# Performance work log

Measured on AMD Instinct MI355X. Metric: run time of the kernel, lower is better.

Reference implementation:

```python
import jax, jax.numpy as jnp
import numpy as np

A_COEF, B_COEF, C_COEF = 1.0, 0.1, 10.0
KL_COEF = 0.005
EPS = 1e-6

B, P1, F, P2 = 32, 778, 1538, 3000
PARAM_DIM, LATENT = 61, 64


def setup_inputs() -> dict:
    key = jax.random.key(0)
    ks = jax.random.split(key, 9)
    return {
        "recon_x": jax.random.normal(ks[0], (B, PARAM_DIM), jnp.float32),
        "x": jax.random.normal(ks[1], (B, PARAM_DIM), jnp.float32),
        "mu": jax.random.normal(ks[2], (B, LATENT), jnp.float32),
        "logvar": jax.random.normal(ks[3], (B, LATENT), jnp.float32),
        "recon_xyz": jax.random.normal(ks[4], (B, P1, 3), jnp.float32),
        "hand_xyz": jax.random.normal(ks[5], (B, P1, 3), jnp.float32),
        "hand_faces": jax.random.randint(ks[6], (B, F, 3), 0, P1, jnp.int64),
        "obj_pts": jax.random.normal(ks[7], (B, P2, 3), jnp.float32),
        "v_weights": jax.random.uniform(ks[8], (P1,), jnp.float32),
    }


def _verts_normals_single(verts, faces):
    # verts: (V,3), faces: (F,3). PyTorch3D-style area-weighted vertex normals.
    v0 = verts[faces[:, 0]]
    v1 = verts[faces[:, 1]]
    v2 = verts[faces[:, 2]]
    fn = jnp.cross(v1 - v0, v2 - v0)  # (F,3) ~ 2*area*face_normal
    n = (jnp.zeros_like(verts)
         .at[faces[:, 0]].add(fn)
         .at[faces[:, 1]].add(fn)
         .at[faces[:, 2]].add(fn))
    norm = jnp.linalg.norm(n, axis=-1, keepdims=True)
    return n / jnp.maximum(norm, EPS)


_verts_normals = jax.vmap(_verts_normals_single)


def _sqdist(xp, yp):
    # (B,P1,P2) pairwise squared distances
    x2 = jnp.sum(xp * xp, axis=-1)[:, :, None]
    y2 = jnp.sum(yp * yp, axis=-1)[:, None, :]
    return x2 + y2 - 2.0 * jnp.einsum('bpd,bqd->bpq', xp, yp)


def _point2point_signed(xp, yp, x_normals):
    # xp: (B,P1,3) hand, yp: (B,P2,3) object, x_normals: (B,P1,3)
    d2 = _sqdist(xp, yp)
    xidx = jnp.argmin(d2, axis=2)  # (B,P1) nearest object point per hand vert
    yidx = jnp.argmin(d2, axis=1)  # (B,P2) nearest hand vert per object point
    x_near = jnp.take_along_axis(yp, xidx[..., None], axis=1)  # (B,P1,3)
    y_near = jnp.take_along_axis(xp, yidx[..., None], axis=1)  # (B,P2,3)
    x2y = xp - x_near
    y2x = yp - y_near
    y_nn = jnp.take_along_axis(x_normals, yidx[..., None], axis=1)  # (B,P2,3)
    in_out = jnp.sign(jnp.sum(y_nn * y2x, axis=-1))
    y2x_signed = jnp.linalg.norm(y2x, axis=2) * in_out  # (B,P2)
    x2y_signed = jnp.linalg.norm(x2y, axis=2)           # (B,P1)
    return y2x_signed, x2y_signed


def _loss_cnet(verts_rhand, verts_rhand_gt, faces, verts_obj, v_weights):
    v_w2 = jnp.power(v_weights, 1.0 / 2.5)
    rh_n = _verts_normals(verts_rhand, faces)
    rh_n_gt = _verts_normals(verts_rhand_gt, faces)
    o2h, h2o = _point2point_signed(verts_rhand, verts_obj, rh_n)
    o2h_gt, h2o_gt = _point2point_signed(verts_rhand_gt, verts_obj, rh_n_gt)
    w_dist = (o2h_gt < 0.01) & (o2h_gt > -0.005)
    w_neg = o2h < 0.0
    w = jnp.where(w_neg, 1.5, jnp.where(w_dist, 1.0, 0.1))
    loss_h = 35.0 * (1.0 - KL_COEF) * jnp.mean(jnp.abs(jnp.abs(h2o) - jnp.abs(h2o_gt)) * v_w2)
    loss_o = 30.0 * (1.0 - KL_COEF) * jnp.mean(jnp.abs(o2h - o2h_gt) * w)
    return loss_h + loss_o


def reference(recon_x, x, mu, logvar, recon_xyz, hand_xyz, hand_faces, obj_pts, v_weights):
    bsz = recon_x.shape[0]
    param_loss = jnp.sum((recon_x - x) ** 2) / bsz
    recon_loss = jnp.sum((recon_xyz - hand_xyz) ** 2) / hand_xyz.shape[0]
    KLD = -0.5 * jnp.sum(1.0 + logvar - mu ** 2 - jnp.exp(logvar)) / hand_xyz.shape[0]
    cvae_loss = recon_loss + KLD
    ho_loss = _loss_cnet(recon_xyz, hand_xyz, hand_faces, obj_pts, v_weights)
    loss = A_COEF * cvae_loss + B_COEF * param_loss + C_COEF * ho_loss
    return loss, param_loss, ho_loss, recon_loss, KLD
```

## Files before the change

### kernel.cpp

```cpp
#include <hip/hip_runtime.h>
#include <math.h>

#define B 32
#define P1 778
#define NF 1538
#define P2 3000
#define PARAM_DIM 61
#define LATENT 64

#define NCH_O2H 4
#define CH_O2H 768
#define NCH_H2O 15
#define CH_H2O 200
#define RED1_BLKS 16
#define HC_BLKS 128
#define OC_BLKS 192
#define HALF_F 769

#define D1_NRM 128
#define D1_TOT (D1_NRM + RED1_BLKS)
#define D2_O2H (NCH_O2H * 64)
#define D2_H2O (NCH_H2O * 64)
#define D2_TOT (D2_O2H + D2_H2O)
#define D3_TOT (OC_BLKS + HC_BLKS)

#define NP_OFF  0
#define NP_SZ   (2*2*B*P1*4)
#define OS_OFF  (NP_OFF + NP_SZ)
#define OS_SZ   (2*B*P2)
#define HP_OFF  (OS_OFF + OS_SZ)
#define HP_SZ   (NCH_H2O*2*B*P1)
#define R1_OFF  (HP_OFF + HP_SZ)
#define RH_OFF  (R1_OFF + RED1_BLKS*3)
#define RO_OFF  (RH_OFF + HC_BLKS)

__global__ __launch_bounds__(256) void kd1(
    const float* __restrict__ recon_x, const float* __restrict__ x,
    const float* __restrict__ mu, const float* __restrict__ logvar,
    const float* __restrict__ recon_xyz, const float* __restrict__ hand_xyz,
    const int* __restrict__ faces, float* __restrict__ ws) {
  __shared__ float4 sv[P1];
  __shared__ float sn[4][2336];
  const int tid = threadIdx.x;
  const int bid = blockIdx.x;

  if (bid < D1_NRM) {
    const int half = bid >> 6, r = bid & 63, set = r >> 5, b = r & 31;
    const float* verts = (set == 0 ? recon_xyz : hand_xyz) + b * P1 * 3;
    const int* f = faces + b * NF * 3 + half * HALF_F * 3;
    const int nf = (half == 0) ? HALF_F : (NF - HALF_F);
    for (int i = tid; i < P1; i += 256)
      sv[i] = make_float4(verts[3*i], verts[3*i+1], verts[3*i+2], 0.f);
    for (int i = tid; i < 4 * 2336; i += 256) ((float*)sn)[i] = 0.f;
    __syncthreads();
    float* s = sn[tid >> 6];
    for (int k = tid; k < nf; k += 256) {
      int i0 = f[3*k], i1 = f[3*k+1], i2 = f[3*k+2];
      float4 v0 = sv[i0], v1 = sv[i1], v2 = sv[i2];
      float e0x = v1.x - v0.x, e0y = v1.y - v0.y, e0z = v1.z - v0.z;
      float e1x = v2.x - v0.x, e1y = v2.y - v0.y, e1z = v2.z - v0.z;
      float fx = e0y * e1z - e0z * e1y;
      float fy = e0z * e1x - e0x * e1z;
      float fz = e0x * e1y - e0y * e1x;
      atomicAdd(&s[3*i0+0], fx); atomicAdd(&s[3*i0+1], fy); atomicAdd(&s[3*i0+2], fz);
      atomicAdd(&s[3*i1+0], fx); atomicAdd(&s[3*i1+1], fy); atomicAdd(&s[3*i1+2], fz);
      atomicAdd(&s[3*i2+0], fx); atomicAdd(&s[3*i2+1], fy); atomicAdd(&s[3*i2+2], fz);
    }
    __syncthreads();
    float4* np = (float4*)(ws + NP_OFF) + (size_t)((half * 2 + set) * B + b) * P1;
    for (int p = tid; p < P1; p += 256) {
      float nx = sn[0][3*p] + sn[1][3*p] + sn[2][3*p] + sn[3][3*p];
      float ny = sn[0][3*p+1] + sn[1][3*p+1] + sn[2][3*p+1] + sn[3][3*p+1];
      float nz = sn[0][3*p+2] + sn[1][3*p+2] + sn[2][3*p+2] + sn[3][3*p+2];
      np[p] = make_float4(nx, ny, nz, 0.f);
    }
  } else {
    const int blk = bid - D1_NRM;
    const int gtid = blk * 256 + tid, stride = RED1_BLKS * 256;
    float sp = 0.f, sr = 0.f, sk = 0.f;
    for (int i = gtid; i < B * PARAM_DIM; i += stride) { float d = recon_x[i] - x[i]; sp += d * d; }
    for (int i = gtid; i < B * P1 * 3; i += stride)    { float d = recon_xyz[i] - hand_xyz[i]; sr += d * d; }
    for (int i = gtid; i < B * LATENT; i += stride)    { float lv = logvar[i], m = mu[i]; sk += 1.f + lv - m * m - expf(lv); }
    for (int off = 32; off > 0; off >>= 1) {
      sp += __shfl_down(sp, off, 64);
      sr += __shfl_down(sr, off, 64);
      sk += __shfl_down(sk, off, 64);
    }
    float* sred = (float*)sn;
    const int wv = tid >> 6;
    if ((tid & 63) == 0) { sred[wv*3] = sp; sred[wv*3+1] = sr; sred[wv*3+2] = sk; }
    __syncthreads();
    if (tid == 0) {
      float a = 0.f, bb = 0.f, c = 0.f;
      for (int w = 0; w < 4; ++w) { a += sred[w*3]; bb += sred[w*3+1]; c += sred[w*3+2]; }
      ws[R1_OFF + blk*3+0] = a; ws[R1_OFF + blk*3+1] = bb; ws[R1_OFF + blk*3+2] = c;
    }
  }
}

__global__ __launch_bounds__(256) void kd2(
    const float* __restrict__ recon_xyz, const float* __restrict__ hand_xyz,
    const float* __restrict__ obj, float* __restrict__ ws) {
  __shared__ float4 s4[P1];
  const int tid = threadIdx.x;
  const int bid = blockIdx.x;

  if (bid < D2_O2H) {
    const int chunk = bid >> 6, r = bid & 63, set = r >> 5, b = r & 31;
    const float* verts = (set == 0 ? recon_xyz : hand_xyz) + b * P1 * 3;
    for (int i = tid; i < P1; i += 256) {
      float vx = verts[3*i], vy = verts[3*i+1], vz = verts[3*i+2];
      s4[i] = make_float4(vx, vy, vz, vx*vx + vy*vy + vz*vz + 64.f);
    }
    __syncthreads();
    const int q0 = chunk * CH_O2H + tid;
    const int q1 = q0 + 256;
    const int q2 = q0 + 512;
    const bool act2 = q2 < P2;
    const float* op = obj + (size_t)b * P2 * 3;
    float p0x = op[3*q0], p0y = op[3*q0+1], p0z = op[3*q0+2];
    float p1x = op[3*q1], p1y = op[3*q1+1], p1z = op[3*q1+2];
    float p2x = 0.f, p2y = 0.f, p2z = 0.f;
    if (act2) { p2x = op[3*q2]; p2y = op[3*q2+1]; p2z = op[3*q2+2]; }
    const float a0 = -2.f*p0x, b0 = -2.f*p0y, c0 = -2.f*p0z;
    const float a1 = -2.f*p1x, b1 = -2.f*p1y, c1 = -2.f*p1z;
    const float a2 = -2.f*p2x, b2 = -2.f*p2y, c2 = -2.f*p2z;
    unsigned best0 = 0xFFFFFFFFu, best1 = 0xFFFFFFFFu, best2 = 0xFFFFFFFFu;
    #pragma unroll 4
    for (int p = 0; p < P1; p += 2) {
      float4 h0 = s4[p], h1 = s4[p+1];
      float d00 = fmaf(h0.x, a0, fmaf(h0.y, b0, fmaf(h0.z, c0, h0.w)));
      float d01 = fmaf(h1.x, a0, fmaf(h1.y, b0, fmaf(h1.z, c0, h1.w)));
      float d10 = fmaf(h0.x, a1, fmaf(h0.y, b1, fmaf(h0.z, c1, h0.w)));
      float d11 = fmaf(h1.x, a1, fmaf(h1.y, b1, fmaf(h1.z, c1, h1.w)));
      float d20 = fmaf(h0.x, a2, fmaf(h0.y, b2, fmaf(h0.z, c2, h0.w)));
      float d21 = fmaf(h1.x, a2, fmaf(h1.y, b2, fmaf(h1.z, c2, h1.w)));
      unsigned k00 = (__float_as_uint(d00) & 0xFFFFFC00u) | (unsigned)p;
      unsigned k01 = (__float_as_uint(d01) & 0xFFFFFC00u) | (unsigned)(p+1);
      unsigned k10 = (__float_as_uint(d10) & 0xFFFFFC00u) | (unsigned)p;
      unsigned k11 = (__float_as_uint(d11) & 0xFFFFFC00u) | (unsigned)(p+1);
      unsigned k20 = (__float_as_uint(d20) & 0xFFFFFC00u) | (unsigned)p;
      unsigned k21 = (__float_as_uint(d21) & 0xFFFFFC00u) | (unsigned)(p+1);
      unsigned n0 = k00 < k01 ? k00 : k01;
      unsigned n1 = k10 < k11 ? k10 : k11;
      unsigned n2 = k20 < k21 ? k20 : k21;
      best0 = n0 < best0 ? n0 : best0;
      best1 = n1 < best1 ? n1 : best1;
      best2 = n2 < best2 ? n2 : best2;
    }
    const float4* np0 = (const float4*)(ws + NP_OFF) + (size_t)(set * B + b) * P1;
    const float4* np1 = np0 + (size_t)2 * B * P1;
    float* os = ws + OS_OFF + (size_t)(set * B + b) * P2;
    {
      int bi = (int)(best0 & 1023u); bi = bi < P1 ? bi : P1 - 1;
      float4 h = s4[bi]; float4 na = np0[bi], nb = np1[bi];
      float nx = na.x + nb.x, ny = na.y + nb.y, nz = na.z + nb.z;
      float dx = p0x - h.x, dy = p0y - h.y, dz = p0z - h.z;
      float d2 = fmaf(dx, dx, fmaf(dy, dy, dz * dz));
      float dt = nx * dx + ny * dy + nz * dz;
      float sg = (dt > 0.f) ? 1.f : ((dt < 0.f) ? -1.f : 0.f);
      os[q0] = sqrtf(d2) * sg;
    }
    {
      int bi = (int)(best1 & 1023u); bi = bi < P1 ? bi : P1 - 1;
      float4 h = s4[bi]; float4 na = np0[bi], nb = np1[bi];
      float nx = na.x + nb.x, ny = na.y + nb.y, nz = na.z + nb.z;
      float dx = p1x - h.x, dy = p1y - h.y, dz = p1z - h.z;
      float d2 = fmaf(dx, dx, fmaf(dy, dy, dz * dz));
      float dt = nx * dx + ny * dy + nz * dz;
      float sg = (dt > 0.f) ? 1.f : ((dt < 0.f) ? -1.f : 0.f);
      os[q1] = sqrtf(d2) * sg;
    }
    if (act2) {
      int bi = (int)(best2 & 1023u); bi = bi < P1 ? bi : P1 - 1;
      float4 h = s4[bi]; float4 na = np0[bi], nb = np1[bi];
      float nx = na.x + nb.x, ny = na.y + nb.y, nz = na.z + nb.z;
      float dx = p2x - h.x, dy = p2y - h.y, dz = p2z - h.z;
      float d2 = fmaf(dx, dx, fmaf(dy, dy, dz * dz));
      float dt = nx * dx + ny * dy + nz * dz;
      float sg = (dt > 0.f) ? 1.f : ((dt < 0.f) ? -1.f : 0.f);
      os[q2] = sqrtf(d2) * sg;
    }

  } else {
    const int t = bid - D2_O2H;
    const int chunk = t >> 6, r = t & 63, set = r >> 5, b = r & 31;
    const float* verts = (set == 0 ? recon_xyz : hand_xyz) + b * P1 * 3;
    const float* op = obj + (size_t)(b * P2 + chunk * CH_H2O) * 3;
    for (int i = tid; i < CH_H2O; i += 256) {
      float ox = op[3*i], oy = op[3*i+1], oz = op[3*i+2];
      s4[i] = make_float4(ox, oy, oz, ox*ox + oy*oy + oz*oz);
    }
    __syncthreads();
    float* part = ws + HP_OFF + (size_t)((chunk * 2 + set) * B + b) * P1;
    const int p0 = tid, p1 = tid + 256, p2 = tid + 512;
    float ax = verts[3*p0], ay = verts[3*p0+1], az = verts[3*p0+2];
    float bx = verts[3*p1], by = verts[3*p1+1], bz = verts[3*p1+2];
    float cx = verts[3*p2], cy = verts[3*p2+1], cz = verts[3*p2+2];
    float h2a = ax*ax+ay*ay+az*az, h2b = bx*bx+by*by+bz*bz, h2c = cx*cx+cy*cy+cz*cz;
    float nax = -2.f*ax, nay = -2.f*ay, naz = -2.f*az;
    float nbx = -2.f*bx, nby = -2.f*by, nbz = -2.f*bz;
    float ncx = -2.f*cx, ncy = -2.f*cy, ncz = -2.f*cz;
    float m0 = 3.0e38f, m1 = 3.0e38f, m2 = 3.0e38f;
    #pragma unroll 4
    for (int qq = 0; qq < CH_H2O; ++qq) {
      float4 o = s4[qq];
      m0 = fminf(m0, fmaf(o.x, nax, fmaf(o.y, nay, fmaf(o.z, naz, o.w))));
      m1 = fminf(m1, fmaf(o.x, nbx, fmaf(o.y, nby, fmaf(o.z, nbz, o.w))));
      m2 = fminf(m2, fmaf(o.x, ncx, fmaf(o.y, ncy, fmaf(o.z, ncz, o.w))));
    }
    part[p0] = m0 + h2a;
    part[p1] = m1 + h2b;
    part[p2] = m2 + h2c;
    if (tid < P1 - 768) {
      const int p3 = 768 + tid;
      float tx = verts[3*p3], ty = verts[3*p3+1], tz = verts[3*p3+2];
      float h2t = tx*tx+ty*ty+tz*tz;
      float ntx = -2.f*tx, nty = -2.f*ty, ntz = -2.f*tz;
      float m3 = 3.0e38f;
      for (int qq = 0; qq < CH_H2O; ++qq) {
        float4 o = s4[qq];
        m3 = fminf(m3, fmaf(o.x, ntx, fmaf(o.y, nty, fmaf(o.z, ntz, o.w))));
      }
      part[p3] = m3 + h2t;
    }
  }
}

__global__ __launch_bounds__(256) void kd3(const float* __restrict__ vw,
                                           float* __restrict__ ws) {
  __shared__ float sred[4];
  const int tid = threadIdx.x;
  const int bid = blockIdx.x;
  if (bid < OC_BLKS) {
    const int gtid = bid * 256 + tid, stride = OC_BLKS * 256;
    float so = 0.f;
    for (int i = gtid; i < B * P2; i += stride) {
      float osA = ws[OS_OFF + i];
      float osB = ws[OS_OFF + (size_t)B * P2 + i];
      bool wdist = (osB < 0.01f) && (osB > -0.005f);
      float w = (osA < 0.f) ? 1.5f : (wdist ? 1.f : 0.1f);
      so += fabsf(osA - osB) * w;
    }
    for (int off = 32; off > 0; off >>= 1) so += __shfl_down(so, off, 64);
    if ((tid & 63) == 0) sred[tid >> 6] = so;
    __syncthreads();
    if (tid == 0) ws[RO_OFF + bid] = sred[0] + sred[1] + sred[2] + sred[3];
  } else {
    const int blk = bid - OC_BLKS;
    const int gtid = blk * 256 + tid, stride = HC_BLKS * 256;
    float sh = 0.f;
    for (int i = gtid; i < B * P1; i += stride) {
      const int p = i % P1;
      float m0 = 3.0e38f, m1 = 3.0e38f;
      #pragma unroll
      for (int c = 0; c < NCH_H2O; ++c) {
        m0 = fminf(m0, ws[HP_OFF + (size_t)(c*2+0) * B * P1 + i]);
        m1 = fminf(m1, ws[HP_OFF + (size_t)(c*2+1) * B * P1 + i]);
      }
      m0 = fmaxf(m0, 0.f); m1 = fmaxf(m1, 0.f);
      sh += fabsf(sqrtf(m0) - sqrtf(m1)) * powf(vw[p], 0.4f);
    }
    for (int off = 32; off > 0; off >>= 1) sh += __shfl_down(sh, off, 64);
    if ((tid & 63) == 0) sred[tid >> 6] = sh;
    __syncthreads();
    if (tid == 0) ws[RH_OFF + blk] = sred[0] + sred[1] + sred[2] + sred[3];
  }
}

__global__ void kfin(const float* __restrict__ ws, float* __restrict__ out) {
  const int lane = threadIdx.x;
  float sp = 0.f, sr = 0.f, sk = 0.f, sh = 0.f, so = 0.f;
  for (int i = lane; i < RED1_BLKS; i += 64) {
    sp += ws[R1_OFF + i*3+0]; sr += ws[R1_OFF + i*3+1]; sk += ws[R1_OFF + i*3+2];
  }
  for (int i = lane; i < HC_BLKS; i += 64) sh += ws[RH_OFF + i];
  for (int i = lane; i < OC_BLKS; i += 64) so += ws[RO_OFF + i];
  for (int off = 32; off > 0; off >>= 1) {
    sp += __shfl_down(sp, off, 64);
    sr += __shfl_down(sr, off, 64);
    sk += __shfl_down(sk, off, 64);
    sh += __shfl_down(sh, off, 64);
    so += __shfl_down(so, off, 64);
  }
  if (lane == 0) {
    float param_loss = sp / (float)B;
    float recon_loss = sr / (float)B;
    float KLD = -0.5f * sk / (float)B;
    float cvae = recon_loss + KLD;
    float loss_h = 35.f * (1.f - 0.005f) * sh / (float)(B * P1);
    float loss_o = 30.f * (1.f - 0.005f) * so / (float)(B * P2);
    float ho = loss_h + loss_o;
    out[0] = cvae + 0.1f * param_loss + 10.f * ho;
    out[1] = param_loss;
    out[2] = ho;
    out[3] = recon_loss;
    out[4] = KLD;
  }
}

extern "C" void kernel_launch(void* const* d_in, const int* in_sizes, int n_in,
                              void* d_out, int out_size, void* d_ws, size_t ws_size,
                              hipStream_t stream) {
  const float* recon_x   = (const float*)d_in[0];
  const float* x         = (const float*)d_in[1];
  const float* mu        = (const float*)d_in[2];
  const float* logvar    = (const float*)d_in[3];
  const float* recon_xyz = (const float*)d_in[4];
  const float* hand_xyz  = (const float*)d_in[5];
  const int*   faces     = (const int*)d_in[6];
  const float* obj       = (const float*)d_in[7];
  const float* vw        = (const float*)d_in[8];
  float* ws = (float*)d_ws;
  float* out = (float*)d_out;

  kd1<<<dim3(D1_TOT), 256, 0, stream>>>(recon_x, x, mu, logvar,
                                        recon_xyz, hand_xyz, faces, ws);
  kd2<<<dim3(D2_TOT), 256, 0, stream>>>(recon_xyz, hand_xyz, obj, ws);
  kd3<<<dim3(D3_TOT), 256, 0, stream>>>(vw, ws);
  kfin<<<1, 64, 0, stream>>>(ws, out);
}
```

Baseline: 129.0 us.

## Compute vertex normals with one face per thread and global atomics

Replaces the shared-memory normal accumulation (2 half-face blocks per mesh, with zeroing and a reduction pass) with one thread per face across 7 chunks per mesh, accumulating directly into global memory with atomics. This removes the second partial-normal buffer and the merge in kd2, and adds a memset of the normal buffer before kd1. It also doubles the scalar-reduction block count. The trade is more global atomic traffic and an extra memset launch in exchange for more parallelism and less per-block setup.

```diff
diff --git a/kernel.cpp b/kernel.cpp
--- a/kernel.cpp
+++ b/kernel.cpp
@@ -12,12 +12,14 @@
 #define CH_O2H 768
 #define NCH_H2O 15
 #define CH_H2O 200
-#define RED1_BLKS 16
+#define RED1_BLKS 32
 #define HC_BLKS 128
 #define OC_BLKS 192
-#define HALF_F 769
-
-#define D1_NRM 128
+
+#define NCH_F 6
+#undef NCH_F
+#define NCH_F 7
+#define D1_NRM (NCH_F * 64)
 #define D1_TOT (D1_NRM + RED1_BLKS)
 #define D2_O2H (NCH_O2H * 64)
 #define D2_H2O (NCH_H2O * 64)
@@ -25,7 +27,7 @@
 #define D3_TOT (OC_BLKS + HC_BLKS)
 
 #define NP_OFF  0
-#define NP_SZ   (2*2*B*P1*4)
+#define NP_SZ   (2*B*P1*4)
 #define OS_OFF  (NP_OFF + NP_SZ)
 #define OS_SZ   (2*B*P2)
 #define HP_OFF  (OS_OFF + OS_SZ)
@@ -39,42 +41,32 @@
     const float* __restrict__ mu, const float* __restrict__ logvar,
     const float* __restrict__ recon_xyz, const float* __restrict__ hand_xyz,
     const int* __restrict__ faces, float* __restrict__ ws) {
-  __shared__ float4 sv[P1];
-  __shared__ float sn[4][2336];
   const int tid = threadIdx.x;
   const int bid = blockIdx.x;
 
   if (bid < D1_NRM) {
-    const int half = bid >> 6, r = bid & 63, set = r >> 5, b = r & 31;
-    const float* verts = (set == 0 ? recon_xyz : hand_xyz) + b * P1 * 3;
-    const int* f = faces + b * NF * 3 + half * HALF_F * 3;
-    const int nf = (half == 0) ? HALF_F : (NF - HALF_F);
-    for (int i = tid; i < P1; i += 256)
-      sv[i] = make_float4(verts[3*i], verts[3*i+1], verts[3*i+2], 0.f);
-    for (int i = tid; i < 4 * 2336; i += 256) ((float*)sn)[i] = 0.f;
-    __syncthreads();
-    float* s = sn[tid >> 6];
-    for (int k = tid; k < nf; k += 256) {
-      int i0 = f[3*k], i1 = f[3*k+1], i2 = f[3*k+2];
-      float4 v0 = sv[i0], v1 = sv[i1], v2 = sv[i2];
-      float e0x = v1.x - v0.x, e0y = v1.y - v0.y, e0z = v1.z - v0.z;
-      float e1x = v2.x - v0.x, e1y = v2.y - v0.y, e1z = v2.z - v0.z;
+    const int sb = bid / NCH_F, chunk = bid - sb * NCH_F;
+    const int set = sb >> 5, b = sb & 31;
+    const int k = chunk * 256 + tid;
+    if (k < NF) {
+      const float* verts = (set == 0 ? recon_xyz : hand_xyz) + b * P1 * 3;
+      const int* f = faces + (b * NF + k) * 3;
+      int i0 = f[0], i1 = f[1], i2 = f[2];
+      float v0x = verts[3*i0], v0y = verts[3*i0+1], v0z = verts[3*i0+2];
+      float v1x = verts[3*i1], v1y = verts[3*i1+1], v1z = verts[3*i1+2];
+      float v2x = verts[3*i2], v2y = verts[3*i2+1], v2z = verts[3*i2+2];
+      float e0x = v1x - v0x, e0y = v1y - v0y, e0z = v1z - v0z;
+      float e1x = v2x - v0x, e1y = v2y - v0y, e1z = v2z - v0z;
       float fx = e0y * e1z - e0z * e1y;
       float fy = e0z * e1x - e0x * e1z;
       float fz = e0x * e1y - e0y * e1x;
-      atomicAdd(&s[3*i0+0], fx); atomicAdd(&s[3*i0+1], fy); atomicAdd(&s[3*i0+2], fz);
-      atomicAdd(&s[3*i1+0], fx); atomicAdd(&s[3*i1+1], fy); atomicAdd(&s[3*i1+2], fz);
-      atomicAdd(&s[3*i2+0], fx); atomicAdd(&s[3*i2+1], fy); atomicAdd(&s[3*i2+2], fz);
-    }
-    __syncthreads();
-    float4* np = (float4*)(ws + NP_OFF) + (size_t)((half * 2 + set) * B + b) * P1;
-    for (int p = tid; p < P1; p += 256) {
-      float nx = sn[0][3*p] + sn[1][3*p] + sn[2][3*p] + sn[3][3*p];
-      float ny = sn[0][3*p+1] + sn[1][3*p+1] + sn[2][3*p+1] + sn[3][3*p+1];
-      float nz = sn[0][3*p+2] + sn[1][3*p+2] + sn[2][3*p+2] + sn[3][3*p+2];
-      np[p] = make_float4(nx, ny, nz, 0.f);
+      float* np = ws + NP_OFF + (size_t)(set * B + b) * P1 * 4;
+      atomicAdd(&np[4*i0+0], fx); atomicAdd(&np[4*i0+1], fy); atomicAdd(&np[4*i0+2], fz);
+      atomicAdd(&np[4*i1+0], fx); atomicAdd(&np[4*i1+1], fy); atomicAdd(&np[4*i1+2], fz);
+      atomicAdd(&np[4*i2+0], fx); atomicAdd(&np[4*i2+1], fy); atomicAdd(&np[4*i2+2], fz);
     }
   } else {
+    __shared__ float sred[12];
     const int blk = bid - D1_NRM;
     const int gtid = blk * 256 + tid, stride = RED1_BLKS * 256;
     float sp = 0.f, sr = 0.f, sk = 0.f;
@@ -86,7 +78,6 @@
       sr += __shfl_down(sr, off, 64);
       sk += __shfl_down(sk, off, 64);
     }
-    float* sred = (float*)sn;
     const int wv = tid >> 6;
     if ((tid & 63) == 0) { sred[wv*3] = sp; sred[wv*3+1] = sr; sred[wv*3+2] = sk; }
     __syncthreads();
@@ -148,36 +139,32 @@
       best1 = n1 < best1 ? n1 : best1;
       best2 = n2 < best2 ? n2 : best2;
     }
-    const float4* np0 = (const float4*)(ws + NP_OFF) + (size_t)(set * B + b) * P1;
-    const float4* np1 = np0 + (size_t)2 * B * P1;
+    const float4* np = (const float4*)(ws + NP_OFF) + (size_t)(set * B + b) * P1;
     float* os = ws + OS_OFF + (size_t)(set * B + b) * P2;
     {
       int bi = (int)(best0 & 1023u); bi = bi < P1 ? bi : P1 - 1;
-      float4 h = s4[bi]; float4 na = np0[bi], nb = np1[bi];
-      float nx = na.x + nb.x, ny = na.y + nb.y, nz = na.z + nb.z;
+      float4 h = s4[bi]; float4 n = np[bi];
       float dx = p0x - h.x, dy = p0y - h.y, dz = p0z - h.z;
       float d2 = fmaf(dx, dx, fmaf(dy, dy, dz * dz));
-      float dt = nx * dx + ny * dy + nz * dz;
+      float dt = n.x * dx + n.y * dy + n.z * dz;
       float sg = (dt > 0.f) ? 1.f : ((dt < 0.f) ? -1.f : 0.f);
       os[q0] = sqrtf(d2) * sg;
     }
     {
       int bi = (int)(best1 & 1023u); bi = bi < P1 ? bi : P1 - 1;
-      float4 h = s4[bi]; float4 na = np0[bi], nb = np1[bi];
-      float nx = na.x + nb.x, ny = na.y + nb.y, nz = na.z + nb.z;
+      float4 h = s4[bi]; float4 n = np[bi];
       float dx = p1x - h.x, dy = p1y - h.y, dz = p1z - h.z;
       float d2 = fmaf(dx, dx, fmaf(dy, dy, dz * dz));
-      float dt = nx * dx + ny * dy + nz * dz;
+      float dt = n.x * dx + n.y * dy + n.z * dz;
       float sg = (dt > 0.f) ? 1.f : ((dt < 0.f) ? -1.f : 0.f);
       os[q1] = sqrtf(d2) * sg;
     }
     if (act2) {
       int bi = (int)(best2 & 1023u); bi = bi < P1 ? bi : P1 - 1;
-      float4 h = s4[bi]; float4 na = np0[bi], nb = np1[bi];
-      float nx = na.x + nb.x, ny = na.y + nb.y, nz = na.z + nb.z;
+      float4 h = s4[bi]; float4 n = np[bi];
       float dx = p2x - h.x, dy = p2y - h.y, dz = p2z - h.z;
       float d2 = fmaf(dx, dx, fmaf(dy, dy, dz * dz));
-      float dt = nx * dx + ny * dy + nz * dz;
+      float dt = n.x * dx + n.y * dy + n.z * dz;
       float sg = (dt > 0.f) ? 1.f : ((dt < 0.f) ? -1.f : 0.f);
       os[q2] = sqrtf(d2) * sg;
     }
@@ -274,8 +261,8 @@
   for (int i = lane; i < RED1_BLKS; i += 64) {
     sp += ws[R1_OFF + i*3+0]; sr += ws[R1_OFF + i*3+1]; sk += ws[R1_OFF + i*3+2];
   }
+  for (int i = lane; i < OC_BLKS; i += 64) so += ws[RO_OFF + i];
   for (int i = lane; i < HC_BLKS; i += 64) sh += ws[RH_OFF + i];
-  for (int i = lane; i < OC_BLKS; i += 64) so += ws[RO_OFF + i];
   for (int off = 32; off > 0; off >>= 1) {
     sp += __shfl_down(sp, off, 64);
     sr += __shfl_down(sr, off, 64);
@@ -314,6 +301,7 @@
   float* ws = (float*)d_ws;
   float* out = (float*)d_out;
 
+  hipMemsetAsync(ws + NP_OFF, 0, NP_SZ * sizeof(float), stream);
   kd1<<<dim3(D1_TOT), 256, 0, stream>>>(recon_x, x, mu, logvar,
                                         recon_xyz, hand_xyz, faces, ws);
   kd2<<<dim3(D2_TOT), 256, 0, stream>>>(recon_xyz, hand_xyz, obj, ws);
```

New measurement: 158.5 us. 1.23x slower.
